# Kernel tuning notes

Measured on AMD Instinct MI355X. Metric: run time of the kernel, lower is better.

## Reference

```python
import jax, jax.numpy as jnp
import numpy as np

B, N, FIN, FOUT, H = 8, 2048, 128, 128, 2


def setup_inputs() -> dict:
    key = jax.random.key(0)
    k_h, k_adj, k_w, k_a = jax.random.split(key, 4)
    h = jax.random.normal(k_h, (B, N, FIN), dtype=jnp.float32)
    adj = jax.random.randint(k_adj, (B, N, N), 0, 2).astype(jnp.int32)
    # self-loops so no softmax row is all -inf
    idx = jnp.arange(N)
    adj = adj.at[:, idx, idx].set(1)
    W = jax.random.normal(k_w, (H, FIN, FOUT), dtype=jnp.float32) * 0.1
    a = jax.random.normal(k_a, (H, 2 * FOUT), dtype=jnp.float32) * 0.1
    return {"h": h, "adj": adj, "W": W, "a": a}


def reference(h, adj, W, a):
    # h: [B,N,FIN], adj: [B,N,N] int, W: [H,FIN,FOUT], a: [H,2*FOUT]
    Fout = W.shape[-1]
    Wh = jnp.einsum('bnf,hfo->bhno', h, W)              # [B,H,N,FOUT]
    # decompose a^T [Wh_i || Wh_j] = a1.Wh_i + a2.Wh_j (exact same math,
    # avoids the [B,N,N,2F] concat the torch code materializes)
    a1, a2 = a[:, :Fout], a[:, Fout:]
    s_i = jnp.einsum('bhno,ho->bhn', Wh, a1)            # score from node i
    s_j = jnp.einsum('bhno,ho->bhn', Wh, a2)            # score from node j
    e = jax.nn.leaky_relu(s_i[:, :, :, None] + s_j[:, :, None, :], 0.2)  # [B,H,N,N]
    e = jnp.where(adj[:, None, :, :] == 0, -jnp.inf, e)
    att = jax.nn.softmax(e, axis=-1)                    # [B,H,N,N]
    out = jnp.einsum('bhnm,bhmo->bhno', att, Wh)        # [B,H,N,FOUT]
    b, hh, n, f = out.shape
    # concat heads along feature dim (head order matches torch cat)
    return out.transpose(0, 2, 1, 3).reshape(b, n, hh * f)
```

## Files before the change

kernel.cpp:

```cpp
#include <hip/hip_runtime.h>
#include <math.h>

constexpr int Bv   = 8;
constexpr int Nv   = 2048;
constexpr int FIN  = 128;
constexpr int FOUT = 128;
constexpr int NH   = 2;
constexpr float LOG2E = 1.44269504088896340736f;

typedef __attribute__((ext_vector_type(8)))  short short8;
typedef __attribute__((ext_vector_type(4)))  float f32x4;
typedef __attribute__((ext_vector_type(16))) float f32x16;
typedef __attribute__((ext_vector_type(4)))  int   i32x4;
typedef unsigned long long u64;

static __device__ __forceinline__ unsigned short f2bf(float f) {
    unsigned u = __builtin_bit_cast(unsigned, f);
    u += 0x7fffu + ((u >> 16) & 1u);
    return (unsigned short)(u >> 16);
}
static __device__ __forceinline__ float bf2f(unsigned short s) {
    unsigned u = ((unsigned)s) << 16;
    return __builtin_bit_cast(float, u);
}
static __device__ __forceinline__ float fast_exp2(float x) {
#if __has_builtin(__builtin_amdgcn_exp2f)
    return __builtin_amdgcn_exp2f(x);
#else
    return exp2f(x);
#endif
}
static __device__ __forceinline__ unsigned cvt_pk_bf16(float lo, float hi) {
    unsigned r;
    asm("v_cvt_pk_bf16_f32 %0, %1, %2" : "=v"(r) : "v"(lo), "v"(hi));
    return r;
}
static __device__ __forceinline__ unsigned bit01(int a) {
    unsigned u = (unsigned)a;
    return u > 1u ? 1u : u;
}

__global__ __launch_bounds__(256) void wa_kernel(const float* __restrict__ W,
                                                 const float* __restrict__ a,
                                                 float* __restrict__ wa,
                                                 unsigned short* __restrict__ wthi,
                                                 unsigned short* __restrict__ wtlo) {
    __shared__ unsigned short shi[FIN * 132];
    __shared__ unsigned short slo[FIN * 132];
    int hh = blockIdx.x;
    int t = threadIdx.x;

    const float* Ws = W + (size_t)hh * FIN * FOUT;
    for (int idx = t; idx < FIN * FOUT; idx += 256) {
        int f = idx >> 7, o = idx & 127;
        float wv = Ws[idx];
        unsigned short uh = f2bf(wv);
        shi[o * 132 + f] = uh;
        slo[o * 132 + f] = f2bf(wv - bf2f(uh));
    }

    int f = t >> 1, half = t & 1;
    const float* Wr = Ws + (size_t)f * FOUT + half * 64;
    const float* ar = a + (size_t)hh * 2 * FOUT + half * 64;
    float s1 = 0.f, s2 = 0.f;
    for (int o = 0; o < 64; o += 4) {
        float4 w4 = *(const float4*)&Wr[o];
        s1 += w4.x * ar[o] + w4.y * ar[o + 1] + w4.z * ar[o + 2] + w4.w * ar[o + 3];
        s2 += w4.x * ar[FOUT + o] + w4.y * ar[FOUT + o + 1] + w4.z * ar[FOUT + o + 2] + w4.w * ar[FOUT + o + 3];
    }
    s1 += __shfl_xor(s1, 1, 64);
    s2 += __shfl_xor(s2, 1, 64);
    if (half == 0) {
        wa[(hh * 2 + 0) * FIN + f] = s1 * LOG2E;
        wa[(hh * 2 + 1) * FIN + f] = s2 * LOG2E;
    }

    __syncthreads();
    unsigned short* dhi = wthi + (size_t)hh * FOUT * FIN;
    unsigned short* dlo = wtlo + (size_t)hh * FOUT * FIN;
    for (int idx = t; idx < FIN * FOUT; idx += 256) {
        int o = idx >> 7, ff = idx & 127;
        dhi[idx] = shi[o * 132 + ff];
        dlo[idx] = slo[o * 132 + ff];
    }
}

__global__ __launch_bounds__(256, 4) void pack_kernel(const int* __restrict__ adj,
                                                      u64* __restrict__ adjp) {
    __shared__ unsigned mlds[8][65];

    int bid = blockIdx.x;
    int t   = threadIdx.x;
    int wv  = t >> 6, l = t & 63;
    int gb  = bid >> 8;
    int r0  = (bid & 255) * 8;

    const int* rp0 = adj + ((size_t)gb * Nv + r0 + wv * 2 + 0) * Nv + l * 32;
    const int* rp1 = adj + ((size_t)gb * Nv + r0 + wv * 2 + 1) * Nv + l * 32;

    int4 av0[8], av1[8];
#pragma unroll
    for (int c = 0; c < 8; ++c) av0[c] = *(const int4*)&rp0[c * 4];
#pragma unroll
    for (int c = 0; c < 8; ++c) av1[c] = *(const int4*)&rp1[c * 4];

    unsigned m0 = 0, m1 = 0;
#pragma unroll
    for (int c = 0; c < 8; ++c) {
        m0 |= bit01(av0[c].x) << (c * 4 + 0);
        m0 |= bit01(av0[c].y) << (c * 4 + 1);
        m0 |= bit01(av0[c].z) << (c * 4 + 2);
        m0 |= bit01(av0[c].w) << (c * 4 + 3);
        m1 |= bit01(av1[c].x) << (c * 4 + 0);
        m1 |= bit01(av1[c].y) << (c * 4 + 1);
        m1 |= bit01(av1[c].z) << (c * 4 + 2);
        m1 |= bit01(av1[c].w) << (c * 4 + 3);
    }
    mlds[wv * 2 + 0][l] = m0;
    mlds[wv * 2 + 1][l] = m1;
    __syncthreads();

    int tt = t >> 3, r = t & 7;
    u64 v = (u64)mlds[r][tt * 2] | ((u64)mlds[r][tt * 2 + 1] << 32);
    adjp[((size_t)gb * 32 + tt) * Nv + r0 + r] = v;
}

__global__ __launch_bounds__(256, 4) void prep2_kernel(
    const float* __restrict__ h, const float* __restrict__ wa,
    const unsigned short* __restrict__ wthi, const unsigned short* __restrict__ wtlo,
    unsigned short* __restrict__ whf, float* __restrict__ si, float* __restrict__ sj) {
    int bid = blockIdx.x;
    int t   = threadIdx.x;

    if (bid < 4096) {
        int row  = bid * 4 + (t >> 6);
        int lane = t & 63;
        float x0 = h[(size_t)row * FIN + lane];
        float x1 = h[(size_t)row * FIN + 64 + lane];
        float s[4];
#pragma unroll
        for (int q = 0; q < 4; ++q) {
            const float* wp = wa + q * FIN;
            s[q] = x0 * wp[lane] + x1 * wp[64 + lane];
        }
#pragma unroll
        for (int m = 32; m >= 1; m >>= 1) {
#pragma unroll
            for (int q = 0; q < 4; ++q) s[q] += __shfl_xor(s[q], m, 64);
        }
        if (lane == 0) {
            int bb = row >> 11, n = row & (Nv - 1);
            si[((size_t)(bb * NH + 0)) * Nv + n] = s[0];
            sj[((size_t)(bb * NH + 0)) * Nv + n] = s[1];
            si[((size_t)(bb * NH + 1)) * Nv + n] = s[2];
            sj[((size_t)(bb * NH + 1)) * Nv + n] = s[3];
        }
    } else {
        int wb2 = bid - 4096;
        int bb  = wb2 & 7;
        int r2  = wb2 >> 3;
        int hh  = r2 & 1;
        int jtb = r2 >> 1;
        int n0  = jtb * 64;

        int w = t >> 6, l = t & 63, lo16 = l & 15, grp = l >> 4;
        int o0 = w * 32;

        const unsigned short* Whi = wthi + (size_t)hh * FOUT * FIN;
        const unsigned short* Wlo = wtlo + (size_t)hh * FOUT * FIN;
        short8 ahi[2][4], alo[2][4];
#pragma unroll
        for (int ot = 0; ot < 2; ++ot)
#pragma unroll
            for (int kt = 0; kt < 4; ++kt) {
                int off = (o0 + ot * 16 + lo16) * FIN + kt * 32 + grp * 8;
                ahi[ot][kt] = *(const short8*)&Whi[off];
                alo[ot][kt] = *(const short8*)&Wlo[off];
            }

        f32x4 acc[2][4];
#pragma unroll
        for (int ot = 0; ot < 2; ++ot)
#pragma unroll
            for (int nt = 0; nt < 4; ++nt) acc[ot][nt] = (f32x4){0.f, 0.f, 0.f, 0.f};

        const float* hb = h + ((size_t)bb * Nv + n0) * FIN;
#pragma unroll
        for (int nt = 0; nt < 4; ++nt) {
#pragma unroll
            for (int kt = 0; kt < 4; ++kt) {
                const float* hp = hb + (size_t)(nt * 16 + lo16) * FIN + kt * 32 + grp * 8;
                float4 x0 = *(const float4*)hp;
                float4 x1 = *(const float4*)(hp + 4);
                float xs[8] = {x0.x, x0.y, x0.z, x0.w, x1.x, x1.y, x1.z, x1.w};
                short8 bhi, blo;
#pragma unroll
                for (int i = 0; i < 8; ++i) {
                    unsigned short uh = f2bf(xs[i]);
                    bhi[i] = (short)uh;
                    blo[i] = (short)f2bf(xs[i] - bf2f(uh));
                }
#pragma unroll
                for (int ot = 0; ot < 2; ++ot) {
                    acc[ot][nt] = __builtin_amdgcn_mfma_f32_16x16x32_bf16(ahi[ot][kt], bhi, acc[ot][nt], 0, 0, 0);
                    acc[ot][nt] = __builtin_amdgcn_mfma_f32_16x16x32_bf16(ahi[ot][kt], blo, acc[ot][nt], 0, 0, 0);
                    acc[ot][nt] = __builtin_amdgcn_mfma_f32_16x16x32_bf16(alo[ot][kt], bhi, acc[ot][nt], 0, 0, 0);
                }
            }
        }
        unsigned short* db = whf + (size_t)(bb * NH + hh) * 262144;
#pragma unroll
        for (int ot = 0; ot < 2; ++ot)
#pragma unroll
            for (int nt = 0; nt < 4; ++nt)
#pragma unroll
                for (int reg = 0; reg < 4; ++reg) {
                    int oc = ot * 16 + grp * 4 + reg;
                    db[(size_t)(((jtb * 4 + nt) * 4 + w) * 64 + (lo16 >> 3) * 32 + oc) * 8 + (lo16 & 7)] =
                        f2bf(acc[ot][nt][reg]);
                }
    }
}

__global__ __launch_bounds__(256, 3) void gat_attn_kernel(
    const u64* __restrict__ adjp, const unsigned short* __restrict__ whf,
    const float* __restrict__ si, const float* __restrict__ sj,
    float* __restrict__ out) {
    int bid = blockIdx.x;
    int bb  = bid & 7;
    int r2  = bid >> 3;
    int rp  = r2 & 31;
    int hh  = (r2 >> 5) & 1;
    int ch  = r2 >> 6;

    int t = threadIdx.x, w = t >> 6, l = t & 63;
    int jp = w & 1, rw = w >> 1;
    int lo32 = l & 31, kh = l >> 5;
    int r0 = rp * 64 + rw * 32;
    int myrow = r0 + lo32;

    float sir = si[(size_t)(bb * NH + hh) * Nv + myrow];
    const u64*   adjr = adjp + (size_t)bb * 32 * Nv + myrow;
    const float* sjb  = sj + (size_t)(bb * NH + hh) * Nv;
    const unsigned short* wbp = whf + (size_t)(bb * NH + hh) * 262144 + (size_t)l * 8;

    f32x16 acc0, acc1, accL;
#pragma unroll
    for (int i = 0; i < 16; ++i) { acc0[i] = 0.f; acc1[i] = 0.f; accL[i] = 0.f; }

    const int ones_w = 0x3f803f80;
    short8 onesf = __builtin_bit_cast(short8, (i32x4){ones_w, ones_w, ones_w, ones_w});

    int jt0 = jp * 16;
    u64 mask = adjr[(size_t)jt0 * Nv];
    for (int jtl = 0; jtl < 16; ++jtl) {
        int jt = jt0 + jtl;
        int jb = jt * 64;
        const unsigned short* fb = wbp + (size_t)(jt * 16 + ch * 2) * 512;
        short8 bf[4][2];
#pragma unroll
        for (int kt = 0; kt < 4; ++kt) {
            bf[kt][0] = *(const short8*)(fb + (kt * 4 + 0) * 512);
            bf[kt][1] = *(const short8*)(fb + (kt * 4 + 1) * 512);
        }
        u64 mcur = mask;
        if (jtl < 15) mask = adjr[(size_t)(jt + 1) * Nv];

        short8 af[4];
#pragma unroll
        for (int kt = 0; kt < 4; ++kt) {
            unsigned mb = (unsigned)(mcur >> (kt * 16 + kh * 8)) & 0xFFu;
            const float* sp = &sjb[jb + kt * 16 + kh * 8];
            float4 s0 = *(const float4*)sp;
            float4 s1 = *(const float4*)(sp + 4);
            float x0 = sir + s0.x, x1 = sir + s0.y, x2 = sir + s0.z, x3 = sir + s0.w;
            float x4 = sir + s1.x, x5 = sir + s1.y, x6 = sir + s1.z, x7 = sir + s1.w;
            x0 = fmaxf(x0, 0.2f * x0); x1 = fmaxf(x1, 0.2f * x1);
            x2 = fmaxf(x2, 0.2f * x2); x3 = fmaxf(x3, 0.2f * x3);
            x4 = fmaxf(x4, 0.2f * x4); x5 = fmaxf(x5, 0.2f * x5);
            x6 = fmaxf(x6, 0.2f * x6); x7 = fmaxf(x7, 0.2f * x7);
            float p0 = fast_exp2(x0), p1 = fast_exp2(x1), p2 = fast_exp2(x2), p3 = fast_exp2(x3);
            float p4 = fast_exp2(x4), p5 = fast_exp2(x5), p6 = fast_exp2(x6), p7 = fast_exp2(x7);
            p0 = (mb & 1u)   ? p0 : 0.f;  p1 = (mb & 2u)   ? p1 : 0.f;
            p2 = (mb & 4u)   ? p2 : 0.f;  p3 = (mb & 8u)   ? p3 : 0.f;
            p4 = (mb & 16u)  ? p4 : 0.f;  p5 = (mb & 32u)  ? p5 : 0.f;
            p6 = (mb & 64u)  ? p6 : 0.f;  p7 = (mb & 128u) ? p7 : 0.f;
            unsigned w0 = cvt_pk_bf16(p0, p1), w1 = cvt_pk_bf16(p2, p3);
            unsigned w2 = cvt_pk_bf16(p4, p5), w3 = cvt_pk_bf16(p6, p7);
            af[kt] = __builtin_bit_cast(short8, (i32x4){(int)w0, (int)w1, (int)w2, (int)w3});
        }
#pragma unroll
        for (int kt = 0; kt < 4; ++kt) {
            acc0 = __builtin_amdgcn_mfma_f32_32x32x16_bf16(af[kt], bf[kt][0], acc0, 0, 0, 0);
            acc1 = __builtin_amdgcn_mfma_f32_32x32x16_bf16(af[kt], bf[kt][1], acc1, 0, 0, 0);
            accL = __builtin_amdgcn_mfma_f32_32x32x16_bf16(af[kt], onesf,    accL, 0, 0, 0);
        }
    }

    __shared__ float red[2][64][49];
    if (jp == 1) {
#pragma unroll
        for (int i = 0; i < 16; ++i) {
            red[rw][l][i]      = acc0[i];
            red[rw][l][16 + i] = acc1[i];
            red[rw][l][32 + i] = accL[i];
        }
    }
    __syncthreads();
    if (jp == 0) {
#pragma unroll
        for (int i = 0; i < 16; ++i) {
            acc0[i] += red[rw][l][i];
            acc1[i] += red[rw][l][16 + i];
            accL[i] += red[rw][l][32 + i];
        }
#pragma unroll
        for (int reg = 0; reg < 16; ++reg) {
            int rowc = (reg & 3) + 8 * (reg >> 2) + 4 * kh;
            float linv = 1.0f / accL[reg];
            float* op = out + ((size_t)(bb * Nv + r0 + rowc)) * (NH * FOUT) + hh * FOUT + ch * 64;
            op[lo32]      = acc0[reg] * linv;
            op[32 + lo32] = acc1[reg] * linv;
        }
    }
}

extern "C" void kernel_launch(void* const* d_in, const int* in_sizes, int n_in,
                              void* d_out, int out_size, void* d_ws, size_t ws_size,
                              hipStream_t stream) {
    const float* h   = (const float*)d_in[0];
    const int*   adj = (const int*)d_in[1];
    const float* W   = (const float*)d_in[2];
    const float* a   = (const float*)d_in[3];
    float*       out = (float*)d_out;

    char* ws = (char*)d_ws;
    unsigned short* whf  = (unsigned short*)ws;
    u64*            adjp = (u64*)(ws + 8388608);
    float* si = (float*)(ws + 8388608 + 4194304);
    float* sj = si + (size_t)Bv * NH * Nv;
    float* wa = sj + (size_t)Bv * NH * Nv;
    unsigned short* wthi = (unsigned short*)(wa + NH * 2 * FIN);
    unsigned short* wtlo = wthi + (size_t)NH * FOUT * FIN;

    wa_kernel   <<<dim3(2),    dim3(256), 0, stream>>>(W, a, wa, wthi, wtlo);
    pack_kernel <<<dim3(2048), dim3(256), 0, stream>>>(adj, adjp);
    prep2_kernel<<<dim3(4608), dim3(256), 0, stream>>>(h, wa, wthi, wtlo, whf, si, sj);
    gat_attn_kernel<<<dim3(1024), dim3(256), 0, stream>>>(adjp, whf, si, sj, out);
}
```

Before: 130.8 us.

## Fuse adjacency bit-packing into attention kernel and drop split-K reduction

Removes the separate pack kernel and its global bitmask buffer. Each attention block now packs its 32 rows of the int32 adjacency into shared memory itself, and the four waves split work across heads and feature halves. Each wave loops over all 32 column tiles, so the cross-wave reduction through shared memory goes away. This saves one launch and a global round trip for the mask, in exchange for fewer blocks (512 instead of 1024), longer serial loops per wave, and a large adjacency read at the start of each block that is not overlapped with compute.

```diff
diff --git a/kernel.cpp b/kernel.cpp
--- a/kernel.cpp
+++ b/kernel.cpp
@@ -85,46 +85,6 @@
     }
 }
 
-__global__ __launch_bounds__(256, 4) void pack_kernel(const int* __restrict__ adj,
-                                                      u64* __restrict__ adjp) {
-    __shared__ unsigned mlds[8][65];
-
-    int bid = blockIdx.x;
-    int t   = threadIdx.x;
-    int wv  = t >> 6, l = t & 63;
-    int gb  = bid >> 8;
-    int r0  = (bid & 255) * 8;
-
-    const int* rp0 = adj + ((size_t)gb * Nv + r0 + wv * 2 + 0) * Nv + l * 32;
-    const int* rp1 = adj + ((size_t)gb * Nv + r0 + wv * 2 + 1) * Nv + l * 32;
-
-    int4 av0[8], av1[8];
-#pragma unroll
-    for (int c = 0; c < 8; ++c) av0[c] = *(const int4*)&rp0[c * 4];
-#pragma unroll
-    for (int c = 0; c < 8; ++c) av1[c] = *(const int4*)&rp1[c * 4];
-
-    unsigned m0 = 0, m1 = 0;
-#pragma unroll
-    for (int c = 0; c < 8; ++c) {
-        m0 |= bit01(av0[c].x) << (c * 4 + 0);
-        m0 |= bit01(av0[c].y) << (c * 4 + 1);
-        m0 |= bit01(av0[c].z) << (c * 4 + 2);
-        m0 |= bit01(av0[c].w) << (c * 4 + 3);
-        m1 |= bit01(av1[c].x) << (c * 4 + 0);
-        m1 |= bit01(av1[c].y) << (c * 4 + 1);
-        m1 |= bit01(av1[c].z) << (c * 4 + 2);
-        m1 |= bit01(av1[c].w) << (c * 4 + 3);
-    }
-    mlds[wv * 2 + 0][l] = m0;
-    mlds[wv * 2 + 1][l] = m1;
-    __syncthreads();
-
-    int tt = t >> 3, r = t & 7;
-    u64 v = (u64)mlds[r][tt * 2] | ((u64)mlds[r][tt * 2 + 1] << 32);
-    adjp[((size_t)gb * 32 + tt) * Nv + r0 + r] = v;
-}
-
 __global__ __launch_bounds__(256, 4) void prep2_kernel(
     const float* __restrict__ h, const float* __restrict__ wa,
     const unsigned short* __restrict__ wthi, const unsigned short* __restrict__ wtlo,
@@ -222,25 +182,44 @@
     }
 }
 
-__global__ __launch_bounds__(256, 3) void gat_attn_kernel(
-    const u64* __restrict__ adjp, const unsigned short* __restrict__ whf,
+__global__ __launch_bounds__(256, 2) void gat_mega_kernel(
+    const int* __restrict__ adj, const unsigned short* __restrict__ whf,
     const float* __restrict__ si, const float* __restrict__ sj,
     float* __restrict__ out) {
+    __shared__ u64 mlds[32][33];
+
     int bid = blockIdx.x;
     int bb  = bid & 7;
-    int r2  = bid >> 3;
-    int rp  = r2 & 31;
-    int hh  = (r2 >> 5) & 1;
-    int ch  = r2 >> 6;
+    int rp  = bid >> 3;
+    int r0  = rp * 32;
 
     int t = threadIdx.x, w = t >> 6, l = t & 63;
-    int jp = w & 1, rw = w >> 1;
+
+    {
+        const int* src = adj + ((size_t)bb * Nv + r0 + w * 8) * Nv + l * 32;
+        for (int r = 0; r < 8; ++r) {
+            const int* rowp = src + (size_t)r * Nv;
+            int4 av[8];
+#pragma unroll
+            for (int c = 0; c < 8; ++c) av[c] = *(const int4*)&rowp[c * 4];
+            unsigned m = 0;
+#pragma unroll
+            for (int c = 0; c < 8; ++c) {
+                m |= bit01(av[c].x) << (c * 4 + 0);
+                m |= bit01(av[c].y) << (c * 4 + 1);
+                m |= bit01(av[c].z) << (c * 4 + 2);
+                m |= bit01(av[c].w) << (c * 4 + 3);
+            }
+            ((unsigned*)&mlds[w * 8 + r][0])[l] = m;
+        }
+    }
+    __syncthreads();
+
+    int hh = w >> 1, ch = w & 1;
     int lo32 = l & 31, kh = l >> 5;
-    int r0 = rp * 64 + rw * 32;
     int myrow = r0 + lo32;
 
     float sir = si[(size_t)(bb * NH + hh) * Nv + myrow];
-    const u64*   adjr = adjp + (size_t)bb * 32 * Nv + myrow;
     const float* sjb  = sj + (size_t)(bb * NH + hh) * Nv;
     const unsigned short* wbp = whf + (size_t)(bb * NH + hh) * 262144 + (size_t)l * 8;
 
@@ -251,10 +230,7 @@
     const int ones_w = 0x3f803f80;
     short8 onesf = __builtin_bit_cast(short8, (i32x4){ones_w, ones_w, ones_w, ones_w});
 
-    int jt0 = jp * 16;
-    u64 mask = adjr[(size_t)jt0 * Nv];
-    for (int jtl = 0; jtl < 16; ++jtl) {
-        int jt = jt0 + jtl;
+    for (int jt = 0; jt < 32; ++jt) {
         int jb = jt * 64;
         const unsigned short* fb = wbp + (size_t)(jt * 16 + ch * 2) * 512;
         short8 bf[4][2];
@@ -263,8 +239,7 @@
             bf[kt][0] = *(const short8*)(fb + (kt * 4 + 0) * 512);
             bf[kt][1] = *(const short8*)(fb + (kt * 4 + 1) * 512);
         }
-        u64 mcur = mask;
-        if (jtl < 15) mask = adjr[(size_t)(jt + 1) * Nv];
+        u64 mcur = mlds[lo32][jt];
 
         short8 af[4];
 #pragma unroll
@@ -297,31 +272,13 @@
         }
     }
 
-    __shared__ float red[2][64][49];
-    if (jp == 1) {
-#pragma unroll
-        for (int i = 0; i < 16; ++i) {
-            red[rw][l][i]      = acc0[i];
-            red[rw][l][16 + i] = acc1[i];
-            red[rw][l][32 + i] = accL[i];
-        }
-    }
-    __syncthreads();
-    if (jp == 0) {
-#pragma unroll
-        for (int i = 0; i < 16; ++i) {
-            acc0[i] += red[rw][l][i];
-            acc1[i] += red[rw][l][16 + i];
-            accL[i] += red[rw][l][32 + i];
-        }
-#pragma unroll
-        for (int reg = 0; reg < 16; ++reg) {
-            int rowc = (reg & 3) + 8 * (reg >> 2) + 4 * kh;
-            float linv = 1.0f / accL[reg];
-            float* op = out + ((size_t)(bb * Nv + r0 + rowc)) * (NH * FOUT) + hh * FOUT + ch * 64;
-            op[lo32]      = acc0[reg] * linv;
-            op[32 + lo32] = acc1[reg] * linv;
-        }
+#pragma unroll
+    for (int reg = 0; reg < 16; ++reg) {
+        int rowc = (reg & 3) + 8 * (reg >> 2) + 4 * kh;
+        float linv = 1.0f / accL[reg];
+        float* op = out + ((size_t)(bb * Nv + r0 + rowc)) * (NH * FOUT) + hh * FOUT + ch * 64;
+        op[lo32]      = acc0[reg] * linv;
+        op[32 + lo32] = acc1[reg] * linv;
     }
 }
 
@@ -336,15 +293,13 @@
 
     char* ws = (char*)d_ws;
     unsigned short* whf  = (unsigned short*)ws;
-    u64*            adjp = (u64*)(ws + 8388608);
-    float* si = (float*)(ws + 8388608 + 4194304);
+    float* si = (float*)(ws + 8388608);
     float* sj = si + (size_t)Bv * NH * Nv;
     float* wa = sj + (size_t)Bv * NH * Nv;
     unsigned short* wthi = (unsigned short*)(wa + NH * 2 * FIN);
     unsigned short* wtlo = wthi + (size_t)NH * FOUT * FIN;
 
     wa_kernel   <<<dim3(2),    dim3(256), 0, stream>>>(W, a, wa, wthi, wtlo);
-    pack_kernel <<<dim3(2048), dim3(256), 0, stream>>>(adj, adjp);
     prep2_kernel<<<dim3(4608), dim3(256), 0, stream>>>(h, wa, wthi, wtlo, whf, si, sj);
-    gat_attn_kernel<<<dim3(1024), dim3(256), 0, stream>>>(adjp, whf, si, sj, out);
-}
+    gat_mega_kernel<<<dim3(512), dim3(256), 0, stream>>>(adj, whf, si, sj, out);
+}
```

Result: slower. 135.8 us (+3.8%).
